# Optimization experiments

Measured on AMD Instinct MI355X. Metric: run time of the kernel, lower is better.

The kernel has to match this reference:

```python
import jax, jax.numpy as jnp
import numpy as np
import math
from jax import lax

S = 2048   # layer_size (number of neurons)
T = 384    # timesteps per forward call
ALPHA = 0.15
DT = 0.1
THRESH = -50.0
V_RESET = -70.0
VL = -70.0
GL = 0.025
CM = 0.5
TAU = CM / GL                                   # 20.0
COEF = DT ** ALPHA * math.gamma(2.0 - ALPHA) / CM  # dt^alpha * Gamma(2-alpha) / Cm


def setup_inputs() -> dict:
    key = jax.random.key(0)
    I_old = jax.random.normal(key, (S, T), dtype=jnp.float32)
    # class-level fractional (Grunwald-Letnikov style) weight vector, x=5000
    x = 5000
    nv = np.arange(x - 1)
    w = ((x - nv + 1) ** (1.0 - ALPHA) - (x - nv) ** (1.0 - ALPHA)).astype(np.float32)
    return {"I_old": I_old, "weights": jnp.asarray(w)}


def _forward(I_old, weights):
    S_, T_ = I_old.shape
    dtype = I_old.dtype
    # wr[a] = weights[-a]: the memory weight applied to a delta that is `a` steps old.
    # Original: np.inner(weights[-N+1:], delta_trace) pairs oldest delta with weights[-(N-1)]
    # and the newest delta with weights[-1].
    wr = jnp.concatenate([jnp.zeros((1,), dtype), weights[::-1][:T_].astype(dtype)])  # [T+1]
    jidx = jnp.arange(T_)  # buffer slot j holds the delta appended at global step j

    def step(carry, xs):
        V, buf = carry          # V: [S], buf: [S, T] delta history (slot j = delta of step j)
        n, I_n = xs             # n: scalar step index, I_n: [S]
        # fractional memory term: sum_{j=1}^{n-1} wr[n-j] * delta_j
        ages = n - jidx                                        # [T]
        coeff = jnp.where((ages >= 1) & (jidx >= 1),
                          wr[jnp.clip(ages, 0, T_)], jnp.zeros((), dtype))  # [T]
        memory = buf @ coeff                                   # [S]
        # three update rules depending on the global step counter
        V1 = V + (DT / TAU) * (-V + I_n / GL)                  # N == 1 branch
        V2 = COEF * (-GL * (V - VL) + I_n) + V - memory        # N >= 2 branch
        V_pre = jnp.where(n == 0, jnp.full_like(V, -70.0),
                          jnp.where(n == 1, V1, V2))
        spike = (V - THRESH > 0).astype(dtype)                 # spike uses PREVIOUS V
        reset = lax.stop_gradient(spike * (THRESH - V_RESET))  # detached reset
        V_new = V_pre - reset
        buf = buf.at[:, n].set(V_new - V)                      # append delta (n=0 slot masked out)
        return (V_new, buf), (spike, V_new)

    V0 = jnp.zeros((S_,), dtype)          # V_trace initialized to 0 per neuron
    buf0 = jnp.zeros((S_, T_), dtype)
    (_, _), (spk, trc) = lax.scan(step, (V0, buf0), (jnp.arange(T_), I_old.T))
    return spk.T, trc.T                    # each [S, T]


def reference(I_old, weights):
    return _forward(I_old, weights)
```

## Files before the change

kernel.cpp:

```cpp
#include <hip/hip_runtime.h>
#include <cmath>

#define T_STEPS 384
#define CH 64
#define NCH 6

__device__ __forceinline__ float readlane_f(float v, int l) {
    return __int_as_float(__builtin_amdgcn_readlane(__float_as_int(v), l));
}

__global__ __launch_bounds__(64)
void flif_kernel(const float* __restrict__ I_old, const float* __restrict__ W,
                 float* __restrict__ out, float c1, float c2, float c3, int Stot)
{
    const int s    = blockIdx.x;
    const int lane = threadIdx.x;
    if (s >= Stot) return;

    __shared__ __align__(16) float wtab[T_STEPS];
    __shared__ float ltab[2 * CH];
    __shared__ __align__(16) float dbuf[T_STEPS];

    const float* Irow = I_old + (size_t)s * T_STEPS;
    float Inext = Irow[lane];

    for (int a = lane; a < T_STEPS; a += 64)
        wtab[a] = a ? W[4999 - a] : 0.0f;
    ltab[lane] = 0.0f;
    ltab[64 + lane] = (lane < 63) ? W[4998 - lane] : 0.0f;
    __syncthreads();

    float* out_spk = out + (size_t)s * T_STEPS;
    float* out_trc = out + (size_t)Stot * T_STEPS + (size_t)s * T_STEPS;

    float V = 0.0f;

    for (int c = 0; c < NCH; ++c) {
        const int cb = c * CH;
        const float Ic = Inext;
        if (c + 1 < NCH) Inext = Irow[cb + CH + lane];

        float acc = 0.0f;
        for (int j = 0; j < cb; j += 4) {
            const float4 d4 = *reinterpret_cast<const float4*>(&dbuf[j]);
            const int b = cb + lane - j;
            acc += d4.x * wtab[b];
            acc += d4.y * wtab[b - 1];
            acc += d4.z * wtab[b - 2];
            acc += d4.w * wtab[b - 3];
        }

        float u = fmaf(c3, Ic, c2) - acc;
        const float Vs = V;
        float tc = 0.0f;

        auto step = [&](int i) {
            const float w  = ltab[lane + 63 - i];
            const float t  = readlane_f(u, i);
            const float V2 = fmaf(c1, V, t);
            const float Vn = V2 - ((V > -50.0f) ? 20.0f : 0.0f);
            const float d  = Vn - V;
            u = fmaf(-w, d, u);
            if (lane == i) tc = Vn;
            V = Vn;
        };

        if (c == 0) {
            {
                V = -90.0f;
                if (lane == 0) tc = V;
            }
            {
                const float I1 = readlane_f(Ic, 1);
                const float V1 = fmaf(0.005f, (I1 / 0.025f) - V, V);
                const float Vn = (V > -50.0f) ? (V1 - 20.0f) : V1;
                const float d  = Vn - V;
                u = fmaf(-ltab[lane + 62], d, u);
                if (lane == 1) tc = Vn;
                V = Vn;
            }
            #pragma unroll
            for (int i = 2; i < CH; ++i) step(i);
        } else {
            #pragma unroll
            for (int i = 0; i < CH; ++i) step(i);
        }

        float prev = __shfl_up(tc, 1);
        if (lane == 0) prev = Vs;
        const float spk = (prev > -50.0f) ? 1.0f : 0.0f;
        float d = tc - prev;
        if (c == 0 && lane == 0) d = 0.0f;
        dbuf[cb + lane] = d;
        out_spk[cb + lane] = spk;
        out_trc[cb + lane] = tc;
        __syncthreads();
    }
}

extern "C" void kernel_launch(void* const* d_in, const int* in_sizes, int n_in,
                              void* d_out, int out_size, void* d_ws, size_t ws_size,
                              hipStream_t stream) {
    const float* I = (const float*)d_in[0];
    const float* W = (const float*)d_in[1];
    float* out = (float*)d_out;
    const int S = in_sizes[0] / T_STEPS;

    const double COEF = std::pow(0.1, 0.15) * std::tgamma(1.85) / 0.5;
    const float c3 = (float)COEF;
    const float c1 = (float)(1.0 - COEF * 0.025);
    const float c2 = (float)(COEF * 0.025 * -70.0);

    flif_kernel<<<S, 64, 0, stream>>>(I, W, out, c1, c2, c3, S);
}
```

Before: 87.04 us.

## Use lane-aligned replicated weight tables and prefetch local weights in the serial recurrence

Stores four shifted copies of the memory-weight table in shared memory so each lane can read its weights as aligned float4 loads, replacing the four scalar unaligned LDS reads per iteration in the history dot product. It also keeps a small rotating register window of the intra-chunk weights, loaded eight steps ahead, so the LDS read latency sits outside the dependent 64-step serial chain. Launch bounds now request two blocks per CU. The costs are more shared memory, extra setup loads, and higher register pressure from the prefetch window.

```diff
diff --git a/kernel.cpp b/kernel.cpp
--- a/kernel.cpp
+++ b/kernel.cpp
@@ -4,36 +4,48 @@
 #define T_STEPS 384
 #define CH 64
 #define NCH 6
+#define WREP_STRIDE 392
 
 __device__ __forceinline__ float readlane_f(float v, int l) {
     return __int_as_float(__builtin_amdgcn_readlane(__float_as_int(v), l));
 }
 
-__global__ __launch_bounds__(64)
+__global__ __launch_bounds__(64, 2)
 void flif_kernel(const float* __restrict__ I_old, const float* __restrict__ W,
                  float* __restrict__ out, float c1, float c2, float c3, int Stot)
 {
     const int s    = blockIdx.x;
     const int lane = threadIdx.x;
-    if (s >= Stot) return;
 
-    __shared__ __align__(16) float wtab[T_STEPS];
+    __shared__ __align__(16) float wrep[4 * WREP_STRIDE];
     __shared__ float ltab[2 * CH];
     __shared__ __align__(16) float dbuf[T_STEPS];
 
     const float* Irow = I_old + (size_t)s * T_STEPS;
     float Inext = Irow[lane];
 
-    for (int a = lane; a < T_STEPS; a += 64)
-        wtab[a] = a ? W[4999 - a] : 0.0f;
     ltab[lane] = 0.0f;
     ltab[64 + lane] = (lane < 63) ? W[4998 - lane] : 0.0f;
+    #pragma unroll
+    for (int r2 = 0; r2 < 4; ++r2) {
+        for (int k = lane; k < WREP_STRIDE; k += 64) {
+            const int i = k + r2;
+            wrep[r2 * WREP_STRIDE + k] = (i >= 1 && i <= 383) ? W[4615 + i] : 0.0f;
+        }
+    }
     __syncthreads();
 
     float* out_spk = out + (size_t)s * T_STEPS;
     float* out_trc = out + (size_t)Stot * T_STEPS + (size_t)s * T_STEPS;
 
+    const int rsel = (-lane) & 3;
+    const float* wlane = wrep + rsel * WREP_STRIDE + (384 - lane - rsel);
+
     float V = 0.0f;
+
+    float wpre[8];
+    #pragma unroll
+    for (int k = 0; k < 8; ++k) wpre[k] = ltab[lane + 63 - k];
 
     for (int c = 0; c < NCH; ++c) {
         const int cb = c * CH;
@@ -41,13 +53,15 @@
         if (c + 1 < NCH) Inext = Irow[cb + CH + lane];
 
         float acc = 0.0f;
+        const float* wp = wlane - cb;
+        #pragma unroll 4
         for (int j = 0; j < cb; j += 4) {
             const float4 d4 = *reinterpret_cast<const float4*>(&dbuf[j]);
-            const int b = cb + lane - j;
-            acc += d4.x * wtab[b];
-            acc += d4.y * wtab[b - 1];
-            acc += d4.z * wtab[b - 2];
-            acc += d4.w * wtab[b - 3];
+            const float4 w4 = *reinterpret_cast<const float4*>(wp + j);
+            acc = fmaf(d4.x, w4.x, acc);
+            acc = fmaf(d4.y, w4.y, acc);
+            acc = fmaf(d4.z, w4.z, acc);
+            acc = fmaf(d4.w, w4.w, acc);
         }
 
         float u = fmaf(c3, Ic, c2) - acc;
@@ -55,10 +69,12 @@
         float tc = 0.0f;
 
         auto step = [&](int i) {
-            const float w  = ltab[lane + 63 - i];
+            const float w = wpre[i & 7];
+            wpre[i & 7] = ltab[lane + 63 - ((i + 8) & 63)];
             const float t  = readlane_f(u, i);
+            const float r  = (V > -50.0f) ? 20.0f : 0.0f;
             const float V2 = fmaf(c1, V, t);
-            const float Vn = V2 - ((V > -50.0f) ? 20.0f : 0.0f);
+            const float Vn = V2 - r;
             const float d  = Vn - V;
             u = fmaf(-w, d, u);
             if (lane == i) tc = Vn;
@@ -67,15 +83,19 @@
 
         if (c == 0) {
             {
+                wpre[0] = ltab[lane + 63 - 8];
                 V = -90.0f;
                 if (lane == 0) tc = V;
             }
             {
+                const float w = wpre[1];
+                wpre[1] = ltab[lane + 63 - 9];
                 const float I1 = readlane_f(Ic, 1);
                 const float V1 = fmaf(0.005f, (I1 / 0.025f) - V, V);
-                const float Vn = (V > -50.0f) ? (V1 - 20.0f) : V1;
+                const float r  = (V > -50.0f) ? 20.0f : 0.0f;
+                const float Vn = V1 - r;
                 const float d  = Vn - V;
-                u = fmaf(-ltab[lane + 62], d, u);
+                u = fmaf(-w, d, u);
                 if (lane == 1) tc = Vn;
                 V = Vn;
             }
```

Measured after the change: 87.69 us. No clear change (+0.7%).
